# Kernel optimization log

Measured on AMD Instinct MI355X. Metric: run time of the kernel, lower is better.

The kernel has to match this reference:

```python
import jax, jax.numpy as jnp
import numpy as np

N_P = 50000   # number of 'place' nodes
N_A = 50000   # number of 'a_transition' nodes
E = 1600000   # edges per edge type
IN = 128      # input feature dim
OUT = 64      # HANConv out_channels
H = 4         # heads
D = OUT // H  # per-head dim
HID = 64      # decoder hidden
NEG_SLOPE = 0.2  # HANConv leaky_relu slope


def setup_inputs() -> dict:
    key = jax.random.key(0)
    ks = jax.random.split(key, 24)
    def nrm(i, shape, scale=1.0):
        return jax.random.normal(ks[i], shape, dtype=jnp.float32) * scale
    w = lambda i, shape, fan: nrm(i, shape, (1.0 / fan) ** 0.5)
    return {
        "x_place": nrm(0, (N_P, IN)),
        "x_atrans": nrm(1, (N_A, IN)),
        "e_pa_src": jax.random.randint(ks[2], (E,), 0, N_P),
        "e_pa_dst": jax.random.randint(ks[3], (E,), 0, N_A),
        "e_aa_src": jax.random.randint(ks[4], (E,), 0, N_A),
        "e_aa_dst": jax.random.randint(ks[5], (E,), 0, N_A),
        "e_ap_src": jax.random.randint(ks[6], (E,), 0, N_A),
        "e_ap_dst": jax.random.randint(ks[7], (E,), 0, N_P),
        "Wp_place": w(8, (IN, OUT), IN),
        "bp_place": jnp.zeros((OUT,), jnp.float32),
        "Wp_atrans": w(9, (IN, OUT), IN),
        "bp_atrans": jnp.zeros((OUT,), jnp.float32),
        "asrc_pa": w(10, (H, D), D),
        "adst_pa": w(11, (H, D), D),
        "asrc_aa": w(12, (H, D), D),
        "adst_aa": w(13, (H, D), D),
        "asrc_ap": w(14, (H, D), D),
        "adst_ap": w(15, (H, D), D),
        "Wk": w(16, (OUT, OUT), OUT),
        "bk": jnp.zeros((OUT,), jnp.float32),
        "q": w(17, (OUT,), OUT),
        "Wd1": w(18, (OUT, HID), OUT),
        "bd1": jnp.zeros((HID,), jnp.float32),
        "Wd2": w(19, (HID, 1), HID),
        "bd2": jnp.zeros((1,), jnp.float32),
    }


def _edge_conv(h_src, h_dst, a_src, a_dst, src, dst, n_dst):
    """HANConv node-level attention for one edge type.
    h_src: [N_src, H, D], h_dst: [N_dst, H, D]; returns relu-aggregated [n_dst, H*D]."""
    alpha = (h_src * a_src).sum(-1)[src] + (h_dst * a_dst).sum(-1)[dst]  # [E, H]
    alpha = jax.nn.leaky_relu(alpha, NEG_SLOPE)
    amax = jax.ops.segment_max(alpha, dst, num_segments=n_dst)
    amax = jnp.where(jnp.isfinite(amax), amax, 0.0)  # guard empty neighborhoods
    ex = jnp.exp(alpha - amax[dst])
    den = jax.ops.segment_sum(ex, dst, num_segments=n_dst) + 1e-16  # PyG softmax eps
    wgt = ex / den[dst]                           # scatter-softmax per dst node [E, H]
    msg = h_src[src] * wgt[:, :, None]            # [E, H, D]
    out = jax.ops.segment_sum(msg, dst, num_segments=n_dst)
    return jax.nn.relu(out.reshape(n_dst, H * D))


def _semantic(outs, q, Wk, bk):
    """HANConv semantic-level attention over edge-type embeddings."""
    stk = jnp.stack(outs)                                       # [T, N, OUT]
    score = (q * jnp.tanh(stk @ Wk + bk).mean(axis=1)).sum(-1)  # [T]
    attn = jax.nn.softmax(score)
    return jnp.einsum('t,tnc->nc', attn, stk)


def reference(x_place, x_atrans, e_pa_src, e_pa_dst, e_aa_src, e_aa_dst, e_ap_src, e_ap_dst,
              Wp_place, bp_place, Wp_atrans, bp_atrans,
              asrc_pa, adst_pa, asrc_aa, adst_aa, asrc_ap, adst_ap,
              Wk, bk, q, Wd1, bd1, Wd2, bd2):
    # per-node-type projection, split into heads
    h_p = (x_place @ Wp_place + bp_place).reshape(N_P, H, D)
    h_a = (x_atrans @ Wp_atrans + bp_atrans).reshape(N_A, H, D)
    # node-level attention per edge type
    out_pa = _edge_conv(h_p, h_a, asrc_pa, adst_pa, e_pa_src, e_pa_dst, N_A)
    out_aa = _edge_conv(h_a, h_a, asrc_aa, adst_aa, e_aa_src, e_aa_dst, N_A)
    out_ap = _edge_conv(h_a, h_p, asrc_ap, adst_ap, e_ap_src, e_ap_dst, N_P)
    # semantic-level attention per destination node type
    x_a = _semantic([out_pa, out_aa], q, Wk, bk)   # 'a_transition'
    _xp = _semantic([out_ap], q, Wk, bk)           # 'place' (computed by encoder, unused downstream)
    # decoder MLP on 'a_transition' + softmax over nodes (dim=0)
    z = jax.nn.relu(x_a @ Wd1 + bd1) @ Wd2 + bd2   # [N_A, 1]
    return jax.nn.softmax(z, axis=0)
```

## Files before the change

kernel.cpp:

```cpp
#include <hip/hip_runtime.h>
#include <hip/hip_fp16.h>
#include <math.h>

#define NP 50000
#define NA 50000
#define NE 1600000
#define IN_DIM 128
#define OUT_DIM 64

#define NB 391
#define BCAP 4608
#define P1_CHUNK 4096
#define P1_GRID ((NE + P1_CHUNK - 1) / P1_CHUNK)
#define PROJ_BLOCKS ((NP + 63) / 64)

typedef _Float16 v8h __attribute__((ext_vector_type(8)));
typedef _Float16 h2f __attribute__((ext_vector_type(2)));
typedef float    v4f __attribute__((ext_vector_type(4)));

__device__ inline float fast_tanh(float x) {
    const float e = __expf(2.f * x);
    return 1.f - 2.f / (e + 1.f);
}

__global__ __launch_bounds__(256) void front_kernel(
    const float* __restrict__ xA, const float* __restrict__ WA, const float* __restrict__ bA,
    const float* __restrict__ xB, const float* __restrict__ WB, const float* __restrict__ bB,
    const float* __restrict__ a_pa_src, const float* __restrict__ a_pa_dst,
    const float* __restrict__ a_aa_src, const float* __restrict__ a_aa_dst,
    ushort* __restrict__ hA, ushort* __restrict__ hB,
    float* __restrict__ s_p_src_pa, float* __restrict__ s_a_dst_pa,
    float* __restrict__ s_a_src_aa, float* __restrict__ s_a_dst_aa,
    const int* __restrict__ srcA, const int* __restrict__ dstA,
    const int* __restrict__ srcB, const int* __restrict__ dstB,
    int* __restrict__ gpart, int* __restrict__ gcur)
{
    __shared__ __align__(16) char smem[22656];
    const int type = blockIdx.y;
    const int tid = threadIdx.x;

    if (blockIdx.x < P1_GRID) {
        const int* src = type ? srcB : srcA;
        const int* dst = type ? dstB : dstA;
        const int ebase = blockIdx.x * P1_CHUNK;
        const int ecount = min(P1_CHUNK, NE - ebase);

        int* hist   = (int*)smem;
        int* starts = hist + NB;
        int* offs2  = starts + NB;
        int* gbase  = offs2 + NB;
        int* sorted = gbase + NB;

        for (int i = tid; i < NB; i += 256) hist[i] = 0;
        __syncthreads();
        for (int i = tid; i < ecount; i += 256)
            atomicAdd(&hist[dst[ebase + i] >> 7], 1);
        __syncthreads();
        if (tid < 64) {
            int carry = 0;
            for (int r = 0; r < 7; ++r) {
                const int idx = r * 64 + tid;
                const int v = (idx < NB) ? hist[idx] : 0;
                int s = v;
                #pragma unroll
                for (int off = 1; off < 64; off <<= 1) {
                    const int t = __shfl_up(s, off);
                    if (tid >= off) s += t;
                }
                if (idx < NB) { starts[idx] = carry + s - v; offs2[idx] = carry + s - v; }
                carry += __shfl(s, 63);
            }
        }
        __syncthreads();
        for (int i = tid; i < ecount; i += 256) {
            const int d = dst[ebase + i];
            const int s = src[ebase + i];
            const int pos = atomicAdd(&offs2[d >> 7], 1);
            sorted[pos] = ((d & 127) << 16) | s;
        }
        __syncthreads();
        for (int b = tid; b < NB; b += 256) {
            const int cnt = hist[b];
            const int flatb = type * NB + b;
            gbase[b] = cnt ? (flatb * BCAP + atomicAdd(&gcur[flatb], cnt)) : 0;
        }
        __syncthreads();
        const int wid = tid >> 6, lane = tid & 63;
        for (int b = wid; b < NB; b += 4) {
            const int st = starts[b], cnt = hist[b], gb = gbase[b];
            for (int i = lane; i < cnt; i += 64) gpart[gb + i] = sorted[st + i];
        }
        return;
    }

    const int pbid = blockIdx.x - P1_GRID;
    const float* x = type ? xB : xA;
    const float* W = type ? WB : WA;
    const float* bias = type ? bB : bA;
    ushort* h_out  = type ? hB : hA;
    const float* c0 = type ? a_pa_dst : a_pa_src;
    float*       s0 = type ? s_a_dst_pa : s_p_src_pa;
    const float* c1 = type ? a_aa_src : nullptr;
    float*       s1 = type ? s_a_src_aa : nullptr;
    const float* c2 = type ? a_aa_dst : nullptr;
    float*       s2 = type ? s_a_dst_aa : nullptr;

    _Float16 (*Wt)[136] = (_Float16(*)[136])smem;
    {
        const float4* W4 = (const float4*)W;
        #pragma unroll
        for (int i = 0; i < 8; ++i) {
            const int f4i = tid + 256 * i;
            const float4 w = W4[f4i];
            const int k = f4i >> 4, c4 = (f4i & 15) * 4;
            Wt[c4 + 0][k] = (_Float16)w.x;
            Wt[c4 + 1][k] = (_Float16)w.y;
            Wt[c4 + 2][k] = (_Float16)w.z;
            Wt[c4 + 3][k] = (_Float16)w.w;
        }
    }
    __syncthreads();

    const int lane = tid & 63;
    const int wid = tid >> 6;
    const int node0 = (pbid * 4 + wid) * 16;
    if (node0 >= NP) return;
    const int m = lane & 15;
    const int quad = lane >> 4;

    v4f acc[4] = {};
    #pragma unroll
    for (int kc = 0; kc < 4; ++kc) {
        const int k0 = kc * 32 + quad * 8;
        const float4 xa = *(const float4*)(x + (size_t)(node0 + m) * IN_DIM + k0);
        const float4 xb2 = *(const float4*)(x + (size_t)(node0 + m) * IN_DIM + k0 + 4);
        v8h af;
        af[0] = (_Float16)xa.x;  af[1] = (_Float16)xa.y;
        af[2] = (_Float16)xa.z;  af[3] = (_Float16)xa.w;
        af[4] = (_Float16)xb2.x; af[5] = (_Float16)xb2.y;
        af[6] = (_Float16)xb2.z; af[7] = (_Float16)xb2.w;
        #pragma unroll
        for (int cb = 0; cb < 4; ++cb) {
            const v8h bf = *(const v8h*)&Wt[cb * 16 + m][k0];
            acc[cb] = __builtin_amdgcn_mfma_f32_16x16x32_f16(af, bf, acc[cb], 0, 0, 0);
        }
    }

    #pragma unroll
    for (int cb = 0; cb < 4; ++cb) {
        const int c = cb * 16 + m;
        const float bv = bias[c];
        float hv[4];
        #pragma unroll
        for (int r = 0; r < 4; ++r) {
            hv[r] = acc[cb][r] + bv;
            const int node = node0 + quad * 4 + r;
            h_out[(size_t)node * 64 + c] = __half_as_ushort(__float2half_rn(hv[r]));
        }
        #define DO_SCORE(A, S)                                         \
            if (A) {                                                   \
                const float av = (A)[c];                               \
                float v0 = hv[0]*av, v1 = hv[1]*av, v2 = hv[2]*av, v3 = hv[3]*av; \
                for (int msk = 1; msk <= 8; msk <<= 1) {               \
                    v0 += __shfl_xor(v0, msk);                         \
                    v1 += __shfl_xor(v1, msk);                         \
                    v2 += __shfl_xor(v2, msk);                         \
                    v3 += __shfl_xor(v3, msk);                         \
                }                                                      \
                if (m == 0) {                                          \
                    const int nb = node0 + quad * 4;                   \
                    (S)[(nb + 0) * 4 + cb] = v0;                       \
                    (S)[(nb + 1) * 4 + cb] = v1;                       \
                    (S)[(nb + 2) * 4 + cb] = v2;                       \
                    (S)[(nb + 3) * 4 + cb] = v3;                       \
                }                                                      \
            }
        DO_SCORE(c0, s0)
        DO_SCORE(c1, s1)
        DO_SCORE(c2, s2)
        #undef DO_SCORE
    }
}

__global__ __launch_bounds__(128) void bscan_kernel(
    const int* __restrict__ gcur, int* __restrict__ bstart)
{
    const int w = threadIdx.x >> 6, lane = threadIdx.x & 63;
    int carry = 0;
    for (int r = 0; r < 7; ++r) {
        const int idx = r * 64 + lane;
        const int flat = w * NB + idx;
        const int v = (idx < NB) ? gcur[flat] : 0;
        int s = v;
        #pragma unroll
        for (int off = 1; off < 64; off <<= 1) {
            const int t = __shfl_up(s, off);
            if (lane >= off) s += t;
        }
        if (idx < NB) bstart[flat] = carry + s - v;
        carry += __shfl(s, 63);
    }
}

__global__ __launch_bounds__(256) void bucket_sort_kernel(
    int* __restrict__ gpart, const int* __restrict__ gcur,
    const int* __restrict__ bstart,
    int* __restrict__ recA, int* __restrict__ offsA,
    int* __restrict__ recB, int* __restrict__ offsB)
{
    const int b = blockIdx.x, type = blockIdx.y;
    int* rec  = type ? recB  : recA;
    int* offs = type ? offsB : offsA;
    const int flat = type * NB + b;
    const int region = flat * BCAP;
    const int cnt = gcur[flat];
    const int bst = bstart[flat];
    const int tid = threadIdx.x;

    __shared__ int hist[128];
    __shared__ int starts[128];
    __shared__ int offs2[128];
    __shared__ int sorted[BCAP];

    if (tid < 128) hist[tid] = 0;
    __syncthreads();
    for (int i = tid; i < cnt; i += 256)
        atomicAdd(&hist[gpart[region + i] >> 16], 1);
    __syncthreads();
    if (tid < 64) {
        int carry = 0;
        for (int r = 0; r < 2; ++r) {
            const int idx = r * 64 + tid;
            const int v = hist[idx];
            int s = v;
            #pragma unroll
            for (int off = 1; off < 64; off <<= 1) {
                const int t = __shfl_up(s, off);
                if (tid >= off) s += t;
            }
            starts[idx] = carry + s - v;
            offs2[idx]  = carry + s - v;
            carry += __shfl(s, 63);
        }
    }
    __syncthreads();
    for (int i = tid; i < cnt; i += 256) {
        const int pk = gpart[region + i];
        const int pos = atomicAdd(&offs2[pk >> 16], 1);
        sorted[pos] = pk & 0xFFFF;
    }
    __syncthreads();
    for (int i = tid; i < cnt; i += 256) rec[bst + i] = sorted[i];
    if (tid < 128) {
        const int n = b * 128 + tid;
        if (n < NA) offs[n] = bst + starts[tid];
    }
    if (b == NB - 1 && tid == 0) offs[NA] = bst + cnt;
}

__global__ __launch_bounds__(256) void gather_kernel(
    const int* __restrict__ offsA, const int* __restrict__ recA,
    const ushort* __restrict__ hA, const float* __restrict__ ssA,
    const float* __restrict__ sdA, float* __restrict__ outA,
    const int* __restrict__ offsB, const int* __restrict__ recB,
    const ushort* __restrict__ hB, const float* __restrict__ ssB,
    const float* __restrict__ sdB, float* __restrict__ outB, int n_dst)
{
    const int type = blockIdx.y;
    const int* offs = type ? offsB : offsA;
    const int* rec  = type ? recB  : recA;
    const ushort* h_src = type ? hB : hA;
    const float* s_src = type ? ssB : ssA;
    const float* s_dst = type ? sdB : sdA;
    float* outbuf = type ? outB : outA;

    const int lane = threadIdx.x & 63;
    const int d = blockIdx.x * 4 + (threadIdx.x >> 6);
    if (d >= n_dst) return;
    const int q = lane & 7;
    const int sub = lane >> 3;
    const int h = q >> 1;
    const float sd = s_dst[d * 4 + h];
    const ushort* hq = h_src + (q << 3);
    const float* ss = s_src + h;
    const int beg = offs[d], end = offs[d + 1];

    float acc[8] = {};
    float wacc = 0.f;
    for (int base = beg; base < end; base += 64) {
        const int c64 = min(64, end - base);
        const int sv = (lane < c64) ? rec[base + lane] : 0;
        const int iters = (c64 + 7) >> 3;
        for (int it = 0; it < iters; ++it) {
            const int idx = it * 8 + sub;
            const int s = __shfl(sv, idx);
            if (idx < c64) {
                float alpha = ss[(size_t)s * 4] + sd;
                alpha = fmaxf(alpha, 0.2f * alpha);
                const float w = __expf(alpha);
                const uint4 pk = *(const uint4*)(hq + ((size_t)s << 6));
                const h2f a0 = __builtin_bit_cast(h2f, pk.x);
                const h2f a1 = __builtin_bit_cast(h2f, pk.y);
                const h2f a2 = __builtin_bit_cast(h2f, pk.z);
                const h2f a3 = __builtin_bit_cast(h2f, pk.w);
                acc[0] = fmaf((float)a0[0], w, acc[0]);
                acc[1] = fmaf((float)a0[1], w, acc[1]);
                acc[2] = fmaf((float)a1[0], w, acc[2]);
                acc[3] = fmaf((float)a1[1], w, acc[3]);
                acc[4] = fmaf((float)a2[0], w, acc[4]);
                acc[5] = fmaf((float)a2[1], w, acc[5]);
                acc[6] = fmaf((float)a3[0], w, acc[6]);
                acc[7] = fmaf((float)a3[1], w, acc[7]);
                wacc += w;
            }
        }
    }
    #pragma unroll
    for (int m = 8; m <= 32; m <<= 1) {
        #pragma unroll
        for (int j = 0; j < 8; ++j) acc[j] += __shfl_xor(acc[j], m);
        wacc += __shfl_xor(wacc, m);
    }
    if (sub == 0) {
        const float inv = 1.f / (wacc + 1e-16f);
        float4 o0, o1;
        o0.x = fmaxf(acc[0] * inv, 0.f);
        o0.y = fmaxf(acc[1] * inv, 0.f);
        o0.z = fmaxf(acc[2] * inv, 0.f);
        o0.w = fmaxf(acc[3] * inv, 0.f);
        o1.x = fmaxf(acc[4] * inv, 0.f);
        o1.y = fmaxf(acc[5] * inv, 0.f);
        o1.z = fmaxf(acc[6] * inv, 0.f);
        o1.w = fmaxf(acc[7] * inv, 0.f);
        float* op = outbuf + (size_t)d * 64 + q * 8;
        *(float4*)op = o0;
        *(float4*)(op + 4) = o1;
    }
}

#define SEM_BLOCKS 512
__global__ __launch_bounds__(256) void semantic_kernel(
    const float* __restrict__ out0, const float* __restrict__ out1,
    const float* __restrict__ Wk, const float* __restrict__ bk,
    float* __restrict__ sem, int n)
{
    __shared__ float Wks[64][64];
    __shared__ float rows[2][4][64];
    const int c = threadIdx.x, ty = threadIdx.y;
    const int tid = ty * 64 + c;
    for (int i = tid; i < 4096; i += 256) ((float*)Wks)[i] = Wk[i];
    const float bkc = bk[c];
    const int ntiles = (n + 3) / 4;
    float acc0 = 0.f, acc1 = 0.f;
    int tile = blockIdx.x;
    float n0 = 0.f, n1 = 0.f;
    {
        const int node = tile * 4 + ty;
        if (node < n) { n0 = out0[(size_t)node * 64 + c]; n1 = out1[(size_t)node * 64 + c]; }
    }
    while (tile < ntiles) {
        __syncthreads();
        rows[0][ty][c] = n0; rows[1][ty][c] = n1;
        __syncthreads();
        const int ntile = tile + gridDim.x;
        if (ntile < ntiles) {
            const int node = ntile * 4 + ty;
            n0 = (node < n) ? out0[(size_t)node * 64 + c] : 0.f;
            n1 = (node < n) ? out1[(size_t)node * 64 + c] : 0.f;
        }
        const int node = tile * 4 + ty;
        if (node < n) {
            float a0 = bkc, a1 = bkc;
            #pragma unroll
            for (int k = 0; k < 64; ++k) {
                const float w = Wks[k][c];
                a0 = fmaf(rows[0][ty][k], w, a0);
                a1 = fmaf(rows[1][ty][k], w, a1);
            }
            acc0 += fast_tanh(a0);
            acc1 += fast_tanh(a1);
        }
        tile = ntile;
    }
    __syncthreads();
    rows[0][ty][c] = acc0; rows[1][ty][c] = acc1;
    __syncthreads();
    if (ty == 0) {
        atomicAdd(&sem[c],      rows[0][0][c] + rows[0][1][c] + rows[0][2][c] + rows[0][3][c]);
        atomicAdd(&sem[64 + c], rows[1][0][c] + rows[1][1][c] + rows[1][2][c] + rows[1][3][c]);
    }
}

__global__ __launch_bounds__(256) void decoder_kernel(
    const float* __restrict__ out0, const float* __restrict__ out1,
    const float* __restrict__ sem, const float* __restrict__ qv,
    const float* __restrict__ Wd1, const float* __restrict__ bd1,
    const float* __restrict__ Wd2, const float* __restrict__ bd2,
    float* __restrict__ z, int n)
{
    __shared__ float xr[4][64];
    __shared__ float attn_s[2];
    const int c = threadIdx.x, ty = threadIdx.y;
    const int node = blockIdx.x * 4 + ty;

    if (ty == 0) {
        float v0 = sem[c] * qv[c];
        float v1 = sem[64 + c] * qv[c];
        for (int off = 32; off >= 1; off >>= 1) {
            v0 += __shfl_xor(v0, off);
            v1 += __shfl_xor(v1, off);
        }
        if (c == 0) {
            const float t0 = v0 / (float)NA, t1 = v1 / (float)NA;
            const float m = fmaxf(t0, t1);
            const float e0 = __expf(t0 - m), e1 = __expf(t1 - m);
            const float inv = 1.f / (e0 + e1);
            attn_s[0] = e0 * inv;
            attn_s[1] = e1 * inv;
        }
    }
    __syncthreads();
    const float a0 = attn_s[0], a1 = attn_s[1];
    if (node < n)
        xr[ty][c] = a0 * out0[(size_t)node * 64 + c] + a1 * out1[(size_t)node * 64 + c];
    __syncthreads();
    if (node >= n) return;
    float acc = bd1[c];
    #pragma unroll
    for (int k = 0; k < 64; ++k)
        acc = fmaf(xr[ty][k], Wd1[k * 64 + c], acc);
    float hv = fmaxf(acc, 0.f) * Wd2[c];
    for (int off = 32; off >= 1; off >>= 1) hv += __shfl_xor(hv, off);
    if (c == 0) z[node] = hv + bd2[0];
}

__global__ __launch_bounds__(256) void softmax_exp_kernel(
    const float* __restrict__ z, float* __restrict__ e,
    float* __restrict__ esum, int n)
{
    float part = 0.f;
    for (int i = blockIdx.x * 256 + threadIdx.x; i < n; i += gridDim.x * 256) {
        const float v = __expf(z[i]);
        e[i] = v;
        part += v;
    }
    for (int off = 32; off >= 1; off >>= 1) part += __shfl_xor(part, off);
    __shared__ float red[4];
    if ((threadIdx.x & 63) == 0) red[threadIdx.x >> 6] = part;
    __syncthreads();
    if (threadIdx.x == 0)
        atomicAdd(esum, red[0] + red[1] + red[2] + red[3]);
}

__global__ __launch_bounds__(256) void softmax_final_kernel(
    const float* __restrict__ e, const float* __restrict__ esum,
    float* __restrict__ out, int n)
{
    const int i = blockIdx.x * 256 + threadIdx.x;
    if (i < n) out[i] = e[i] / (*esum);
}

extern "C" void kernel_launch(void* const* d_in, const int* in_sizes, int n_in,
                              void* d_out, int out_size, void* d_ws, size_t ws_size,
                              hipStream_t stream)
{
    const float* x_place  = (const float*)d_in[0];
    const float* x_atrans = (const float*)d_in[1];
    const int* e_pa_src = (const int*)d_in[2];
    const int* e_pa_dst = (const int*)d_in[3];
    const int* e_aa_src = (const int*)d_in[4];
    const int* e_aa_dst = (const int*)d_in[5];
    const float* Wp_place  = (const float*)d_in[8];
    const float* bp_place  = (const float*)d_in[9];
    const float* Wp_atrans = (const float*)d_in[10];
    const float* bp_atrans = (const float*)d_in[11];
    const float* asrc_pa = (const float*)d_in[12];
    const float* adst_pa = (const float*)d_in[13];
    const float* asrc_aa = (const float*)d_in[14];
    const float* adst_aa = (const float*)d_in[15];
    const float* Wk  = (const float*)d_in[18];
    const float* bk  = (const float*)d_in[19];
    const float* q   = (const float*)d_in[20];
    const float* Wd1 = (const float*)d_in[21];
    const float* bd1 = (const float*)d_in[22];
    const float* Wd2 = (const float*)d_in[23];
    const float* bd2 = (const float*)d_in[24];
    float* out = (float*)d_out;

    float* ws = (float*)d_ws;
    size_t off = 0;
    auto alloc = [&](size_t n) {
        float* p = ws + off; off += (n + 3) & ~(size_t)3; return p;
    };

    ushort* h_p       = (ushort*)alloc((size_t)NP * 32);
    ushort* h_a       = (ushort*)alloc((size_t)NA * 32);
    float* s_p_src_pa = alloc((size_t)NP * 4);
    float* s_a_dst_pa = alloc((size_t)NA * 4);
    float* s_a_src_aa = alloc((size_t)NA * 4);
    float* s_a_dst_aa = alloc((size_t)NA * 4);
    float* out_pa     = alloc((size_t)NA * 64);
    float* out_aa     = alloc((size_t)NA * 64);
    int*   offs_pa    = (int*)alloc(NA + 1);
    int*   offs_aa    = (int*)alloc(NA + 1);
    int*   rec_pa     = (int*)alloc(NE);
    int*   rec_aa     = (int*)alloc(NE);
    int*   gcur       = (int*)alloc(2 * NB);
    float* sem        = alloc(128);
    float* esum       = alloc(4);
    int*   bstart     = (int*)alloc(2 * NB);
    float* zbuf       = alloc(NA);
    float* ebuf       = alloc(NA);
    int* gpart = (int*)out_pa;
    (void)ws_size; (void)in_sizes; (void)n_in; (void)out_size;

    const size_t zbytes = (size_t)((char*)(esum + 4) - (char*)gcur);
    hipMemsetAsync(gcur, 0, zbytes, stream);

    front_kernel<<<dim3(P1_GRID + PROJ_BLOCKS, 2), 256, 0, stream>>>(
        x_place, Wp_place, bp_place,
        x_atrans, Wp_atrans, bp_atrans,
        asrc_pa, adst_pa, asrc_aa, adst_aa,
        h_p, h_a,
        s_p_src_pa, s_a_dst_pa, s_a_src_aa, s_a_dst_aa,
        e_pa_src, e_pa_dst, e_aa_src, e_aa_dst, gpart, gcur);

    bscan_kernel<<<1, 128, 0, stream>>>(gcur, bstart);
    bucket_sort_kernel<<<dim3(NB, 2), 256, 0, stream>>>(
        gpart, gcur, bstart, rec_pa, offs_pa, rec_aa, offs_aa);

    gather_kernel<<<dim3((NA + 3) / 4, 2), 256, 0, stream>>>(
        offs_pa, rec_pa, h_p, s_p_src_pa, s_a_dst_pa, out_pa,
        offs_aa, rec_aa, h_a, s_a_src_aa, s_a_dst_aa, out_aa, NA);

    dim3 b64x4(64, 4);
    semantic_kernel<<<SEM_BLOCKS, b64x4, 0, stream>>>(out_pa, out_aa, Wk, bk, sem, NA);
    decoder_kernel<<<NA / 4, b64x4, 0, stream>>>(
        out_pa, out_aa, sem, q, Wd1, bd1, Wd2, bd2, zbuf, NA);
    softmax_exp_kernel<<<196, 256, 0, stream>>>(zbuf, ebuf, esum, NA);
    softmax_final_kernel<<<(NA + 255) / 256, 256, 0, stream>>>(ebuf, esum, out, NA);
}
```

Baseline: 352.5 us.

## Fold bucket prefix scan into sort, fuse softmax exp into decoder, flatten scatter

Removes the single-block bucket-scan kernel by having each bucket-sort block sum its preceding bucket counts itself. Fuses the exponent and partial-sum step of the softmax into the decoder kernel, with the sum spread over 16 atomic slots, and drops the separate exp kernel. Encodes the bin index into each sorted record so the partition write-out becomes one flat coalesced loop instead of a per-bucket wave loop. Together these cut kernel launches and the serialized small kernels. The cost is redundant reads of bucket counts in every sort block and many more atomics on the softmax sum, and the exp is taken without subtracting a max.

```diff
diff --git a/kernel.cpp b/kernel.cpp
--- a/kernel.cpp
+++ b/kernel.cpp
@@ -49,7 +49,7 @@
         int* starts = hist + NB;
         int* offs2  = starts + NB;
         int* gbase  = offs2 + NB;
-        int* sorted = gbase + NB;
+        unsigned* sorted = (unsigned*)(gbase + NB);
 
         for (int i = tid; i < NB; i += 256) hist[i] = 0;
         __syncthreads();
@@ -75,8 +75,9 @@
         for (int i = tid; i < ecount; i += 256) {
             const int d = dst[ebase + i];
             const int s = src[ebase + i];
-            const int pos = atomicAdd(&offs2[d >> 7], 1);
-            sorted[pos] = ((d & 127) << 16) | s;
+            const int bin = d >> 7;
+            const int pos = atomicAdd(&offs2[bin], 1);
+            sorted[pos] = ((unsigned)bin << 23) | ((unsigned)(d & 127) << 16) | (unsigned)s;
         }
         __syncthreads();
         for (int b = tid; b < NB; b += 256) {
@@ -85,10 +86,10 @@
             gbase[b] = cnt ? (flatb * BCAP + atomicAdd(&gcur[flatb], cnt)) : 0;
         }
         __syncthreads();
-        const int wid = tid >> 6, lane = tid & 63;
-        for (int b = wid; b < NB; b += 4) {
-            const int st = starts[b], cnt = hist[b], gb = gbase[b];
-            for (int i = lane; i < cnt; i += 64) gpart[gb + i] = sorted[st + i];
+        for (int i = tid; i < ecount; i += 256) {
+            const unsigned e = sorted[i];
+            const int bin = e >> 23;
+            gpart[gbase[bin] + (i - starts[bin])] = (int)(e & 0x7FFFFF);
         }
         return;
     }
@@ -182,29 +183,8 @@
     }
 }
 
-__global__ __launch_bounds__(128) void bscan_kernel(
-    const int* __restrict__ gcur, int* __restrict__ bstart)
-{
-    const int w = threadIdx.x >> 6, lane = threadIdx.x & 63;
-    int carry = 0;
-    for (int r = 0; r < 7; ++r) {
-        const int idx = r * 64 + lane;
-        const int flat = w * NB + idx;
-        const int v = (idx < NB) ? gcur[flat] : 0;
-        int s = v;
-        #pragma unroll
-        for (int off = 1; off < 64; off <<= 1) {
-            const int t = __shfl_up(s, off);
-            if (lane >= off) s += t;
-        }
-        if (idx < NB) bstart[flat] = carry + s - v;
-        carry += __shfl(s, 63);
-    }
-}
-
 __global__ __launch_bounds__(256) void bucket_sort_kernel(
     int* __restrict__ gpart, const int* __restrict__ gcur,
-    const int* __restrict__ bstart,
     int* __restrict__ recA, int* __restrict__ offsA,
     int* __restrict__ recB, int* __restrict__ offsB)
 {
@@ -214,16 +194,23 @@
     const int flat = type * NB + b;
     const int region = flat * BCAP;
     const int cnt = gcur[flat];
-    const int bst = bstart[flat];
     const int tid = threadIdx.x;
 
     __shared__ int hist[128];
     __shared__ int starts[128];
     __shared__ int offs2[128];
+    __shared__ int red[4];
     __shared__ int sorted[BCAP];
 
+    int p = 0;
+    for (int i = tid; i < b; i += 256) p += gcur[type * NB + i];
+    #pragma unroll
+    for (int msk = 1; msk <= 32; msk <<= 1) p += __shfl_xor(p, msk);
+    if ((tid & 63) == 0) red[tid >> 6] = p;
     if (tid < 128) hist[tid] = 0;
     __syncthreads();
+    const int bst = red[0] + red[1] + red[2] + red[3];
+
     for (int i = tid; i < cnt; i += 256)
         atomicAdd(&hist[gpart[region + i] >> 16], 1);
     __syncthreads();
@@ -396,10 +383,11 @@
     const float* __restrict__ sem, const float* __restrict__ qv,
     const float* __restrict__ Wd1, const float* __restrict__ bd1,
     const float* __restrict__ Wd2, const float* __restrict__ bd2,
-    float* __restrict__ z, int n)
+    float* __restrict__ ebuf, float* __restrict__ esum, int n)
 {
     __shared__ float xr[4][64];
     __shared__ float attn_s[2];
+    __shared__ float zsh[4];
     const int c = threadIdx.x, ty = threadIdx.y;
     const int node = blockIdx.x * 4 + ty;
 
@@ -419,45 +407,39 @@
             attn_s[1] = e1 * inv;
         }
     }
+    if (c == 0) zsh[ty] = 0.f;
     __syncthreads();
     const float a0 = attn_s[0], a1 = attn_s[1];
     if (node < n)
         xr[ty][c] = a0 * out0[(size_t)node * 64 + c] + a1 * out1[(size_t)node * 64 + c];
     __syncthreads();
-    if (node >= n) return;
-    float acc = bd1[c];
-    #pragma unroll
-    for (int k = 0; k < 64; ++k)
-        acc = fmaf(xr[ty][k], Wd1[k * 64 + c], acc);
-    float hv = fmaxf(acc, 0.f) * Wd2[c];
-    for (int off = 32; off >= 1; off >>= 1) hv += __shfl_xor(hv, off);
-    if (c == 0) z[node] = hv + bd2[0];
-}
-
-__global__ __launch_bounds__(256) void softmax_exp_kernel(
-    const float* __restrict__ z, float* __restrict__ e,
-    float* __restrict__ esum, int n)
-{
-    float part = 0.f;
-    for (int i = blockIdx.x * 256 + threadIdx.x; i < n; i += gridDim.x * 256) {
-        const float v = __expf(z[i]);
-        e[i] = v;
-        part += v;
-    }
-    for (int off = 32; off >= 1; off >>= 1) part += __shfl_xor(part, off);
-    __shared__ float red[4];
-    if ((threadIdx.x & 63) == 0) red[threadIdx.x >> 6] = part;
-    __syncthreads();
-    if (threadIdx.x == 0)
-        atomicAdd(esum, red[0] + red[1] + red[2] + red[3]);
+    if (node < n) {
+        float acc = bd1[c];
+        #pragma unroll
+        for (int k = 0; k < 64; ++k)
+            acc = fmaf(xr[ty][k], Wd1[k * 64 + c], acc);
+        float hv = fmaxf(acc, 0.f) * Wd2[c];
+        for (int off = 32; off >= 1; off >>= 1) hv += __shfl_xor(hv, off);
+        if (c == 0) {
+            const float e = __expf(hv + bd2[0]);
+            ebuf[node] = e;
+            zsh[ty] = e;
+        }
+    }
+    __syncthreads();
+    if (c == 0 && ty == 0)
+        atomicAdd(&esum[blockIdx.x & 15], zsh[0] + zsh[1] + zsh[2] + zsh[3]);
 }
 
 __global__ __launch_bounds__(256) void softmax_final_kernel(
     const float* __restrict__ e, const float* __restrict__ esum,
     float* __restrict__ out, int n)
 {
+    float s = 0.f;
+    #pragma unroll
+    for (int j = 0; j < 16; ++j) s += esum[j];
     const int i = blockIdx.x * 256 + threadIdx.x;
-    if (i < n) out[i] = e[i] / (*esum);
+    if (i < n) out[i] = e[i] / s;
 }
 
 extern "C" void kernel_launch(void* const* d_in, const int* in_sizes, int n_in,
@@ -507,14 +489,12 @@
     int*   rec_aa     = (int*)alloc(NE);
     int*   gcur       = (int*)alloc(2 * NB);
     float* sem        = alloc(128);
-    float* esum       = alloc(4);
-    int*   bstart     = (int*)alloc(2 * NB);
-    float* zbuf       = alloc(NA);
+    float* esum       = alloc(16);
     float* ebuf       = alloc(NA);
     int* gpart = (int*)out_pa;
     (void)ws_size; (void)in_sizes; (void)n_in; (void)out_size;
 
-    const size_t zbytes = (size_t)((char*)(esum + 4) - (char*)gcur);
+    const size_t zbytes = (size_t)((char*)(esum + 16) - (char*)gcur);
     hipMemsetAsync(gcur, 0, zbytes, stream);
 
     front_kernel<<<dim3(P1_GRID + PROJ_BLOCKS, 2), 256, 0, stream>>>(
@@ -525,9 +505,8 @@
         s_p_src_pa, s_a_dst_pa, s_a_src_aa, s_a_dst_aa,
         e_pa_src, e_pa_dst, e_aa_src, e_aa_dst, gpart, gcur);
 
-    bscan_kernel<<<1, 128, 0, stream>>>(gcur, bstart);
     bucket_sort_kernel<<<dim3(NB, 2), 256, 0, stream>>>(
-        gpart, gcur, bstart, rec_pa, offs_pa, rec_aa, offs_aa);
+        gpart, gcur, rec_pa, offs_pa, rec_aa, offs_aa);
 
     gather_kernel<<<dim3((NA + 3) / 4, 2), 256, 0, stream>>>(
         offs_pa, rec_pa, h_p, s_p_src_pa, s_a_dst_pa, out_pa,
@@ -536,7 +515,6 @@
     dim3 b64x4(64, 4);
     semantic_kernel<<<SEM_BLOCKS, b64x4, 0, stream>>>(out_pa, out_aa, Wk, bk, sem, NA);
     decoder_kernel<<<NA / 4, b64x4, 0, stream>>>(
-        out_pa, out_aa, sem, q, Wd1, bd1, Wd2, bd2, zbuf, NA);
-    softmax_exp_kernel<<<196, 256, 0, stream>>>(zbuf, ebuf, esum, NA);
+        out_pa, out_aa, sem, q, Wd1, bd1, Wd2, bd2, ebuf, esum, NA);
     softmax_final_kernel<<<(NA + 255) / 256, 256, 0, stream>>>(ebuf, esum, out, NA);
 }
```

Measured after the change: 551.5 us. 56.4% more time.
